# Optimization experiments

Hardware: AMD Instinct MI355X
Metric: run time of the kernel (lower is better)

Reference implementation:

```python
import jax, jax.numpy as jnp
import numpy as np

GRID_LO = 32
GRID_HI = 128
NF = 4          # n_features
K = 9           # num_neighbors
NUM_CLASSES = 36
BS = 128
P_LO = GRID_LO * GRID_LO   # 1024
P_HI = GRID_HI * GRID_HI   # 16384


def _knn_neighbor_indices():
    """Replicates cKDTree(lo_coords).query(hi_coords, k=K)[1]: lo grid has
    spacing ratio=grid_hi//grid_lo, hi grid spacing 1; neighbors sorted by
    distance (stable sort -> ties broken by lower linear index)."""
    ratio = GRID_HI // GRID_LO
    lo = np.stack(np.meshgrid(np.arange(GRID_LO) * ratio,
                              np.arange(GRID_LO) * ratio, indexing='ij'),
                  axis=-1).reshape(-1, 2).astype(np.float64)   # (P_LO, 2)
    hi = np.stack(np.meshgrid(np.arange(GRID_HI),
                              np.arange(GRID_HI), indexing='ij'),
                  axis=-1).reshape(-1, 2).astype(np.float64)   # (P_HI, 2)
    d2 = ((hi[:, None, :] - lo[None, :, :]) ** 2).sum(-1)      # (P_HI, P_LO)
    idx = np.argsort(d2, axis=1, kind='stable')[:, :K]          # (P_HI, K)
    return jnp.asarray(idx, dtype=jnp.int32)


def setup_inputs() -> dict:
    key = jax.random.key(0)
    k1, k2, k3, k4, k5 = jax.random.split(key, 5)
    x = jax.random.normal(k1, (BS, NF * P_LO), dtype=jnp.float32)
    cls_ids = jax.random.randint(k2, (BS,), 0, NUM_CLASSES)
    neighbor_indices = _knn_neighbor_indices()                  # (P_HI, K)
    weight_map = jax.random.normal(k3, (NUM_CLASSES, NF, P_HI, K), dtype=jnp.float32) * 0.05
    bias_low = jax.random.normal(k4, (NUM_CLASSES, NF, P_LO), dtype=jnp.float32) * 0.05
    bias_high = jax.random.normal(k5, (NUM_CLASSES, NF, P_HI), dtype=jnp.float32) * 0.05
    return {"x": x, "cls_ids": cls_ids, "neighbor_indices": neighbor_indices,
            "weight_map": weight_map, "bias_low": bias_low, "bias_high": bias_high}


def reference(x, cls_ids, neighbor_indices, weight_map, bias_low, bias_high):
    # x: (BS, NF*P_LO) -> (BS, NF, P_LO)
    y_low = x.reshape(x.shape[0], NF, P_LO)
    y_low_db = y_low - bias_low[cls_ids]                        # (BS, NF, P_LO)
    # gather k=9 lo-res neighbors for every hi-res pixel (all features at once)
    neigh = y_low_db[:, :, neighbor_indices]                    # (BS, NF, P_HI, K)
    weights = weight_map[cls_ids]                               # (BS, NF, P_HI, K)
    out = jnp.einsum('bfpk,bfpk->bfp', neigh, weights)          # weighted sum over k
    out = out + bias_high[cls_ids]                              # (BS, NF, P_HI)
    return out.reshape(x.shape[0], NF, GRID_HI, GRID_HI)
```

## Files before the change

kernel.cpp:

```cpp
#include <hip/hip_runtime.h>

#define BS      128
#define NF      4
#define NC      36
#define P_LO    1024
#define P_HI    16384
#define KNN     9
#define THREADS 256
#define TILE_P  512
#define TILE_F  (TILE_P * KNN)
#define NTILES  (P_HI / TILE_P)
#define LIST_OFF 64

__global__ __launch_bounds__(128) void build_lists_kernel(
    const int* __restrict__ cls_ids, int* __restrict__ ws)
{
    __shared__ int cnt[NC];
    const int t = threadIdx.x;
    if (t < NC) cnt[t] = 0;
    __syncthreads();
    if (t < BS) {
        int c = cls_ids[t];
        int pos = atomicAdd(&cnt[c], 1);
        ws[LIST_OFF + c * BS + pos] = t;
    }
    __syncthreads();
    if (t < NC) ws[t] = cnt[t];
}

__global__ __launch_bounds__(THREADS) void rect_up_kernel(
    const float* __restrict__ x,
    const int*   __restrict__ ws,
    const int*   __restrict__ nbr,
    const float* __restrict__ wmap,
    const float* __restrict__ blo,
    const float* __restrict__ bhi,
    float*       __restrict__ out)
{
    __shared__ __align__(16) char smem[TILE_F * 4 * 2];
    float* w_st = (float*)smem;
    int*   i_st = (int*)(smem + TILE_F * 4);
    float* ybuf = (float*)(smem + TILE_F * 4);

    const int tile = blockIdx.x % NTILES;
    const int cf   = blockIdx.x / NTILES;
    const int f    = cf % NF;
    const int cls  = cf / NF;

    const int n_b = ws[cls];
    if (n_b == 0) return;

    const int tid   = threadIdx.x;
    const int tbase = tile * TILE_P;

    const float4* wsrc = (const float4*)(wmap + ((size_t)(cls * NF + f) * P_HI + tbase) * KNN);
    const int4*   isrc = (const int4*)(nbr + (size_t)tbase * KNN);
    float4* w4 = (float4*)w_st;
    int4*   i4 = (int4*)i_st;
    #pragma unroll
    for (int i = tid; i < TILE_F / 4; i += THREADS) {
        w4[i] = wsrc[i];
        i4[i] = isrc[i];
    }
    __syncthreads();

    float w[18]; int nb[18];
    {
        const float2* wr = (const float2*)w_st + (size_t)tid * 9;
        const int2*   ir = (const int2*)i_st + (size_t)tid * 9;
        #pragma unroll
        for (int j = 0; j < 9; ++j) {
            float2 a = wr[j]; w[2 * j] = a.x; w[2 * j + 1] = a.y;
            int2   c = ir[j]; nb[2 * j] = c.x; nb[2 * j + 1] = c.y;
        }
    }
    __syncthreads();

    const int    p0 = tbase + 2 * tid;
    const float2 bh = *(const float2*)(bhi + (size_t)(cls * NF + f) * P_HI + p0);
    const float4 bl = ((const float4*)(blo + (cls * NF + f) * P_LO))[tid];
    const int*  list = ws + LIST_OFF + cls * BS;

    {
        const int b = list[0];
        float4 xv = ((const float4*)(x + (b * NF + f) * P_LO))[tid];
        float4 r;
        r.x = xv.x - bl.x; r.y = xv.y - bl.y;
        r.z = xv.z - bl.z; r.w = xv.w - bl.w;
        ((float4*)ybuf)[tid] = r;
    }

    for (int s = 0; s < n_b; ++s) {
        __syncthreads();
        const float* y = ybuf + (s & 1) * P_LO;
        if (s + 1 < n_b) {
            const int b1 = list[s + 1];
            float4 xv = ((const float4*)(x + (b1 * NF + f) * P_LO))[tid];
            float4 r;
            r.x = xv.x - bl.x; r.y = xv.y - bl.y;
            r.z = xv.z - bl.z; r.w = xv.w - bl.w;
            ((float4*)(ybuf + ((s + 1) & 1) * P_LO))[tid] = r;
        }
        const int b = list[s];
        float a0 = 0.f, a1 = 0.f;
        #pragma unroll
        for (int k = 0; k < 9; ++k) a0 = fmaf(w[k],     y[nb[k]],     a0);
        #pragma unroll
        for (int k = 0; k < 9; ++k) a1 = fmaf(w[9 + k], y[nb[9 + k]], a1);
        float2 o;
        o.x = a0 + bh.x;
        o.y = a1 + bh.y;
        *(float2*)(out + (size_t)(b * NF + f) * P_HI + p0) = o;
    }
}

extern "C" void kernel_launch(void* const* d_in, const int* in_sizes, int n_in,
                              void* d_out, int out_size, void* d_ws, size_t ws_size,
                              hipStream_t stream) {
    const float* x    = (const float*)d_in[0];
    const int*   cls  = (const int*)d_in[1];
    const int*   nbr  = (const int*)d_in[2];
    const float* wmap = (const float*)d_in[3];
    const float* blo  = (const float*)d_in[4];
    const float* bhi  = (const float*)d_in[5];
    float*       out  = (float*)d_out;
    int*         wsl  = (int*)d_ws;

    build_lists_kernel<<<1, 128, 0, stream>>>(cls, wsl);
    rect_up_kernel<<<NC * NF * NTILES, THREADS, 0, stream>>>(
        x, wsl, nbr, wmap, blo, bhi, out);
}
```

Before: 166.3 us.

## Batch four samples per LDS gather pass with async weight/index staging

```diff
diff --git a/kernel.cpp b/kernel.cpp
--- a/kernel.cpp
+++ b/kernel.cpp
@@ -7,8 +7,7 @@
 #define P_HI    16384
 #define KNN     9
 #define THREADS 256
-#define TILE_P  512
-#define TILE_F  (TILE_P * KNN)
+#define TILE_P  256
 #define NTILES  (P_HI / TILE_P)
 #define LIST_OFF 64
 
@@ -28,7 +27,13 @@
     if (t < NC) ws[t] = cnt[t];
 }
 
-__global__ __launch_bounds__(THREADS) void rect_up_kernel(
+__device__ __forceinline__ void async_cp16(const void* g, void* l) {
+    __builtin_amdgcn_global_load_lds(
+        (const __attribute__((address_space(1))) void*)g,
+        (__attribute__((address_space(3))) void*)l, 16, 0, 0);
+}
+
+__global__ __launch_bounds__(THREADS, 8) void rect_up_kernel(
     const float* __restrict__ x,
     const int*   __restrict__ ws,
     const int*   __restrict__ nbr,
@@ -37,10 +42,7 @@
     const float* __restrict__ bhi,
     float*       __restrict__ out)
 {
-    __shared__ __align__(16) char smem[TILE_F * 4 * 2];
-    float* w_st = (float*)smem;
-    int*   i_st = (int*)(smem + TILE_F * 4);
-    float* ybuf = (float*)(smem + TILE_F * 4);
+    __shared__ __align__(16) char smem[2 * TILE_P * KNN * 4];
 
     const int tile = blockIdx.x % NTILES;
     const int cf   = blockIdx.x / NTILES;
@@ -52,65 +54,87 @@
 
     const int tid   = threadIdx.x;
     const int tbase = tile * TILE_P;
+    const int p     = tbase + tid;
 
     const float4* wsrc = (const float4*)(wmap + ((size_t)(cls * NF + f) * P_HI + tbase) * KNN);
-    const int4*   isrc = (const int4*)(nbr + (size_t)tbase * KNN);
-    float4* w4 = (float4*)w_st;
-    int4*   i4 = (int4*)i_st;
-    #pragma unroll
-    for (int i = tid; i < TILE_F / 4; i += THREADS) {
-        w4[i] = wsrc[i];
-        i4[i] = isrc[i];
+    const float4* isrc = (const float4*)(nbr + (size_t)tbase * KNN);
+    float4* wdst = (float4*)smem;
+    float4* idst = (float4*)(smem + TILE_P * KNN * 4);
+    async_cp16(wsrc + tid,       wdst + tid);
+    async_cp16(wsrc + tid + 256, wdst + tid + 256);
+    async_cp16(isrc + tid,       idst + tid);
+    async_cp16(isrc + tid + 256, idst + tid + 256);
+    if (tid < 64) {
+        async_cp16(wsrc + 512 + tid, wdst + 512 + tid);
+        async_cp16(isrc + 512 + tid, idst + 512 + tid);
+    }
+
+    const float* blp = blo + (size_t)(cls * NF + f) * P_LO;
+    float blv0 = blp[tid];
+    float blv1 = blp[tid + 256];
+    float blv2 = blp[tid + 512];
+    float blv3 = blp[tid + 768];
+    const float bh = bhi[(size_t)(cls * NF + f) * P_HI + p];
+    const int* list = ws + LIST_OFF + cls * BS;
+
+    asm volatile("s_waitcnt vmcnt(0)" ::: "memory");
+    __syncthreads();
+
+    float w[KNN]; int nb[KNN];
+    {
+        const float* wrow = (const float*)smem + (size_t)tid * KNN;
+        const int*   irow = (const int*)(smem + TILE_P * KNN * 4) + (size_t)tid * KNN;
+        #pragma unroll
+        for (int k = 0; k < KNN; ++k) { w[k] = wrow[k]; nb[k] = irow[k]; }
     }
     __syncthreads();
 
-    float w[18]; int nb[18];
-    {
-        const float2* wr = (const float2*)w_st + (size_t)tid * 9;
-        const int2*   ir = (const int2*)i_st + (size_t)tid * 9;
+    float4* ybuf = (float4*)smem;
+
+    const int R = (n_b + 3) >> 2;
+    for (int r = 0; r < R; ++r) {
+        const int s0 = 4 * r;
+        const int b0 = list[s0];
+        const int b1 = list[(s0 + 1 < n_b) ? s0 + 1 : n_b - 1];
+        const int b2 = list[(s0 + 2 < n_b) ? s0 + 2 : n_b - 1];
+        const int b3 = list[(s0 + 3 < n_b) ? s0 + 3 : n_b - 1];
+        const float* x0 = x + ((size_t)(b0 * NF + f)) * P_LO;
+        const float* x1 = x + ((size_t)(b1 * NF + f)) * P_LO;
+        const float* x2 = x + ((size_t)(b2 * NF + f)) * P_LO;
+        const float* x3 = x + ((size_t)(b3 * NF + f)) * P_LO;
+
+        if (r) __syncthreads();
+
+        {
+            float blv[4] = {blv0, blv1, blv2, blv3};
+            #pragma unroll
+            for (int m = 0; m < 4; ++m) {
+                const int q = tid + (m << 8);
+                const float bl = blv[m];
+                float4 v;
+                v.x = x0[q] - bl;
+                v.y = x1[q] - bl;
+                v.z = x2[q] - bl;
+                v.w = x3[q] - bl;
+                ybuf[q] = v;
+            }
+        }
+        __syncthreads();
+
+        float a0 = 0.f, a1 = 0.f, a2 = 0.f, a3 = 0.f;
         #pragma unroll
-        for (int j = 0; j < 9; ++j) {
-            float2 a = wr[j]; w[2 * j] = a.x; w[2 * j + 1] = a.y;
-            int2   c = ir[j]; nb[2 * j] = c.x; nb[2 * j + 1] = c.y;
+        for (int k = 0; k < KNN; ++k) {
+            const float4 yv = ybuf[nb[k]];
+            a0 = fmaf(w[k], yv.x, a0);
+            a1 = fmaf(w[k], yv.y, a1);
+            a2 = fmaf(w[k], yv.z, a2);
+            a3 = fmaf(w[k], yv.w, a3);
         }
-    }
-    __syncthreads();
 
-    const int    p0 = tbase + 2 * tid;
-    const float2 bh = *(const float2*)(bhi + (size_t)(cls * NF + f) * P_HI + p0);
-    const float4 bl = ((const float4*)(blo + (cls * NF + f) * P_LO))[tid];
-    const int*  list = ws + LIST_OFF + cls * BS;
-
-    {
-        const int b = list[0];
-        float4 xv = ((const float4*)(x + (b * NF + f) * P_LO))[tid];
-        float4 r;
-        r.x = xv.x - bl.x; r.y = xv.y - bl.y;
-        r.z = xv.z - bl.z; r.w = xv.w - bl.w;
-        ((float4*)ybuf)[tid] = r;
-    }
-
-    for (int s = 0; s < n_b; ++s) {
-        __syncthreads();
-        const float* y = ybuf + (s & 1) * P_LO;
-        if (s + 1 < n_b) {
-            const int b1 = list[s + 1];
-            float4 xv = ((const float4*)(x + (b1 * NF + f) * P_LO))[tid];
-            float4 r;
-            r.x = xv.x - bl.x; r.y = xv.y - bl.y;
-            r.z = xv.z - bl.z; r.w = xv.w - bl.w;
-            ((float4*)(ybuf + ((s + 1) & 1) * P_LO))[tid] = r;
-        }
-        const int b = list[s];
-        float a0 = 0.f, a1 = 0.f;
-        #pragma unroll
-        for (int k = 0; k < 9; ++k) a0 = fmaf(w[k],     y[nb[k]],     a0);
-        #pragma unroll
-        for (int k = 0; k < 9; ++k) a1 = fmaf(w[9 + k], y[nb[9 + k]], a1);
-        float2 o;
-        o.x = a0 + bh.x;
-        o.y = a1 + bh.y;
-        *(float2*)(out + (size_t)(b * NF + f) * P_HI + p0) = o;
+        out[(size_t)(b0 * NF + f) * P_HI + p] = a0 + bh;
+        if (s0 + 1 < n_b) out[(size_t)(b1 * NF + f) * P_HI + p] = a1 + bh;
+        if (s0 + 2 < n_b) out[(size_t)(b2 * NF + f) * P_HI + p] = a2 + bh;
+        if (s0 + 3 < n_b) out[(size_t)(b3 * NF + f) * P_HI + p] = a3 + bh;
     }
 }
 
```

New measurement: 200.7 us. 20.6% more time.
